# Optimization experiments

Measured on AMD Instinct MI355X. Metric: run time of the kernel, lower is better.

## Reference

```python
import jax, jax.numpy as jnp
import numpy as np

N_PROP, N_GRID, N_KEY, C_FEAT = 128, 216, 4096, 128
RADII = (0.8, 1.6)
NSAMPLES = (16, 16)
C_OUT = 64  # per-branch MLP output channels


def setup_inputs() -> dict:
    key = jax.random.key(0)
    ks = jax.random.split(key, 20)
    s = 0.05
    return {
        "wlh": jax.random.uniform(ks[0], (N_PROP, 3)) * 4.0 + 0.5,
        "center": jax.random.normal(ks[1], (N_PROP, 3)) * 5.0,
        "yaw": jax.random.uniform(ks[2], (N_PROP,)) * 2.0 * np.pi,
        "u": jax.random.uniform(ks[3], (N_PROP, N_GRID, 3)),
        "keypoints_xyz": jax.random.normal(ks[4], (1, N_KEY, 3)) * 5.0,
        "keypoints_features": jax.random.normal(ks[5], (1, C_FEAT, N_KEY)),
        "pn0_w1": jax.random.normal(ks[6], (C_OUT, C_FEAT + 3)) * s,
        "pn0_g1": jnp.ones((C_OUT,)), "pn0_b1": jnp.zeros((C_OUT,)),
        "pn0_w2": jax.random.normal(ks[7], (C_OUT, C_OUT)) * s,
        "pn0_g2": jnp.ones((C_OUT,)), "pn0_b2": jnp.zeros((C_OUT,)),
        "pn1_w1": jax.random.normal(ks[8], (C_OUT, C_FEAT + 3)) * s,
        "pn1_g1": jnp.ones((C_OUT,)), "pn1_b1": jnp.zeros((C_OUT,)),
        "pn1_w2": jax.random.normal(ks[9], (C_OUT, C_OUT)) * s,
        "pn1_g2": jnp.ones((C_OUT,)), "pn1_b2": jnp.zeros((C_OUT,)),
        "red_w1": jax.random.normal(ks[10], (256, N_GRID * 2 * C_OUT)) * 0.01,
        "red_b1": jnp.zeros((256,)),
        "red_w2": jax.random.normal(ks[11], (256, 256)) * s,
        "red_b2": jnp.zeros((256,)),
    }


def reference(wlh, center, yaw, u, keypoints_xyz, keypoints_features,
              pn0_w1, pn0_g1, pn0_b1, pn0_w2, pn0_g2, pn0_b2,
              pn1_w1, pn1_g1, pn1_b1, pn1_w2, pn1_g2, pn1_b2,
              red_w1, red_b1, red_w2, red_b2):
    n, m, _ = u.shape
    # --- sample gridpoints inside proposals and rotate by yaw around z ---
    gp = u * wlh[:, None, :]                                 # (n, m, 3)
    c, s = jnp.cos(yaw), jnp.sin(yaw)
    R = jnp.stack([c, -s, s, c], axis=-1).reshape(-1, 2, 2)   # (n, 2, 2)
    xy = jnp.einsum('njk,nmk->nmj', R, gp[..., :2])
    grid = jnp.concatenate([xy, gp[..., 2:]], -1) + center[:, None, :]
    grid = grid.reshape(-1, 3)                               # (G, 3), G = n*m

    kp = keypoints_xyz[0]                                    # (K, 3)
    kf = jnp.transpose(keypoints_features[0])                # (K, C)
    K = kp.shape[0]

    # squared distances (G, K) without materializing (G, K, 3)
    d2 = (jnp.sum(grid * grid, -1)[:, None]
          + jnp.sum(kp * kp, -1)[None, :]
          - 2.0 * grid @ kp.T)

    def ball_query(radius, nsample):
        # first `nsample` in-radius indices in original order; pad with first
        # hit; all-zeros if no point in radius (pointnet2 CUDA semantics).
        mask = d2 < radius * radius
        cand = jnp.where(mask, jnp.arange(K, dtype=jnp.int32), K)
        srt = jnp.sort(cand, axis=-1)[:, :nsample]           # (G, ns)
        first = srt[:, :1]
        return jnp.where(srt < K, srt, jnp.where(first < K, first, 0))

    def branch(radius, nsample, w1, g1, b1, w2, g2, b2):
        idx = ball_query(radius, nsample)                    # (G, ns)
        xyz = kp[idx] - grid[:, None, :]                     # (G, ns, 3)
        x = jnp.concatenate([xyz, kf[idx]], -1)              # (G, ns, 3+C)
        h = jax.nn.relu(jnp.einsum('gnc,oc->gno', x, w1) * g1 + b1)
        h = jax.nn.relu(jnp.einsum('gnc,oc->gno', h, w2) * g2 + b2)
        return jnp.max(h, axis=1)                            # (G, C_OUT)

    f0 = branch(RADII[0], NSAMPLES[0], pn0_w1, pn0_g1, pn0_b1, pn0_w2, pn0_g2, pn0_b2)
    f1 = branch(RADII[1], NSAMPLES[1], pn1_w1, pn1_g1, pn1_b1, pn1_w2, pn1_g2, pn1_b2)
    pooled = jnp.concatenate([f0, f1], -1)                   # (G, 2*C_OUT)
    Cp = pooled.shape[-1]

    # faithful replication of (1,C,n,m).permute(0,3,1,2).view(1,n,-1)
    t = pooled.reshape(n, m, Cp)                             # gridpoint order (n, m)
    red_in = jnp.transpose(t, (1, 2, 0)).reshape(1, n, m * Cp)

    h = jax.nn.relu(red_in @ red_w1.T + red_b1)
    return jax.nn.relu(h @ red_w2.T + red_b2)                # (1, n, 256)
```

## Files before the change

kernel.cpp:

```cpp
#include <hip/hip_runtime.h>
#include <hip/hip_bf16.h>

typedef unsigned short u16;
typedef unsigned int   u32;
typedef unsigned long long u64;

#define N_PROPC 128
#define N_GRIDC 216
#define G_TOT   27648
#define N_KEYC  4096
#define C_FEATC 128
#define R0SQ    0.64f
#define R1SQ    2.56f
#define BF16_ONES_DWORD 0x3F803F80u

typedef __attribute__((ext_vector_type(8))) short bf16x8;
typedef __attribute__((ext_vector_type(4))) float f32x4;

#if __has_builtin(__builtin_amdgcn_fcmpf)
#define BALLOT_LT(a, b) __builtin_amdgcn_fcmpf((a), (b), 4)
#else
#define BALLOT_LT(a, b) __ballot((a) < (b))
#endif

__device__ __forceinline__ float bf2f(u16 u) {
    return __uint_as_float(((u32)u) << 16);
}
__device__ __forceinline__ u16 f2bf(float f) {
    u32 u = __float_as_uint(f);
    u32 r = (u + 0x7fffu + ((u >> 16) & 1u)) >> 16;
    return (u16)r;
}
__device__ __forceinline__ bool is_bf16(const u32* flagp) {
    return *flagp == BF16_ONES_DWORD;
}
__device__ __forceinline__ float ld(const void* p, int i, bool bf) {
    return bf ? bf2f(((const u16*)p)[i]) : ((const float*)p)[i];
}
__device__ __forceinline__ u16 ldb(const void* p, int i, bool bf) {
    return bf ? ((const u16*)p)[i] : f2bf(((const float*)p)[i]);
}

__global__ __launch_bounds__(256) void prep_fused_kernel(
    const u32* __restrict__ flagp,
    const void* __restrict__ kxyz,
    const void* __restrict__ wlh, const void* __restrict__ center,
    const void* __restrict__ yaw, const void* __restrict__ uu,
    const void* __restrict__ kf,
    const void* __restrict__ w10, const void* __restrict__ g10, const void* __restrict__ b10,
    const void* __restrict__ w20, const void* __restrict__ g20, const void* __restrict__ b20,
    const void* __restrict__ w11, const void* __restrict__ g11, const void* __restrict__ b11,
    const void* __restrict__ w21, const void* __restrict__ g21, const void* __restrict__ b21,
    const void* __restrict__ rw2,
    float4* __restrict__ kp4, float4* __restrict__ grid4, u16* __restrict__ kfT,
    u16* __restrict__ w1mf, u16* __restrict__ w2mf,
    float* __restrict__ g1f, float* __restrict__ b1f,
    float* __restrict__ g2f, float* __restrict__ b2f,
    float* __restrict__ w2rT)
{
    const bool bf = is_bf16(flagp);
    const int bid = blockIdx.x, tid = threadIdx.x;

    if (bid < 16) {
        int k = bid * 256 + tid;
        float x = ld(kxyz, k*3, bf), y = ld(kxyz, k*3+1, bf), z = ld(kxyz, k*3+2, bf);
        kp4[k] = make_float4(x, y, z, 0.0f);
    } else if (bid < 124) {
        int g = (bid - 16) * 256 + tid;
        int n = g / N_GRIDC;
        float ux = ld(uu, g*3, bf), uy = ld(uu, g*3+1, bf), uz = ld(uu, g*3+2, bf);
        float gpx = ux * ld(wlh, n*3, bf);
        float gpy = uy * ld(wlh, n*3+1, bf);
        float gpz = uz * ld(wlh, n*3+2, bf);
        float yv = ld(yaw, n, bf);
        float c = cosf(yv), sn = sinf(yv);
        float x = (c*gpx - sn*gpy) + ld(center, n*3, bf);
        float y = (sn*gpx + c*gpy) + ld(center, n*3+1, bf);
        float z = gpz + ld(center, n*3+2, bf);
        grid4[g] = make_float4(x, y, z, 0.0f);
    } else if (bid < 2172) {
        int t = (bid - 124) * 256 + tid;
        int key = t >> 7, feat = t & 127;
        kfT[t] = ldb(kf, feat * N_KEYC + key, bf);
    } else if (bid < 2174) {
        const int b = bid - 2172;
        const void* w1 = b ? w11 : w10; const void* g1v = b ? g11 : g10;
        const void* w2 = b ? w21 : w20; const void* g2v = b ? g21 : g20;
        const void* b1v = b ? b11 : b10; const void* b2v = b ? b21 : b20;
        for (int f = tid; f < 10240; f += 256) {
            int j = f & 7, t1 = f >> 3;
            int n = t1 & 15, t2 = t1 >> 4;
            int quad = t2 & 3, t3 = t2 >> 2;
            int kt = t3 % 5, nt = t3 / 5;
            int k = kt*32 + quad*8 + j;
            int o = nt*16 + n;
            u16 v = 0;
            if (k < 128)      v = ldb(w1, o*131 + 3 + k, bf);
            else if (k < 131) v = ldb(w1, o*131 + (k - 128), bf);
            w1mf[b*10240 + f] = v;
        }
        for (int f = tid; f < 4096; f += 256) {
            int j = f & 7, t1 = f >> 3;
            int n = t1 & 15, t2 = t1 >> 4;
            int quad = t2 & 3, t3 = t2 >> 2;
            int kt = t3 & 1, nt = t3 >> 1;
            int k = kt*32 + quad*8 + j;
            int o = nt*16 + n;
            w2mf[b*4096 + f] = ldb(w2, o*64 + k, bf);
        }
        if (tid < 64) {
            g1f[b*64 + tid] = ld(g1v, tid, bf);
            b1f[b*64 + tid] = ld(b1v, tid, bf);
            g2f[b*64 + tid] = ld(g2v, tid, bf);
            b2f[b*64 + tid] = ld(b2v, tid, bf);
        }
    } else {
        int t = (bid - 2174) * 256 + tid;
        int o = t & 255, c = t >> 8;
        w2rT[c*256 + o] = ld(rw2, o*256 + c, bf);
    }
}

__global__ __launch_bounds__(256) void ballquery_kernel(
    const float4* __restrict__ kp4,
    const float4* __restrict__ grid4, u16* __restrict__ idx01)
{
    __shared__ __attribute__((aligned(16))) float4 sk[2048];
    const int tid = threadIdx.x;
    const int lane = tid & 63;
    const int wid = tid >> 6;
    const int g0 = blockIdx.x * 16 + wid * 4;
    const float4 gra = grid4[g0];
    const float4 grb = grid4[g0 + 1];
    const float4 grc = grid4[g0 + 2];
    const float4 grd = grid4[g0 + 3];

    u64 m0[4] = {0, 0, 0, 0};
    u64 m1[4] = {0, 0, 0, 0};
    #pragma unroll 1
    for (int pass = 0; pass < 2; ++pass) {
        if (pass) __syncthreads();
        for (int t = tid; t < 2048; t += 256) sk[t] = kp4[pass*2048 + t];
        __syncthreads();
        #pragma unroll
        for (int it = 0; it < 32; ++it) {
            const float4 kv = sk[it*64 + lane];
            const int chunk = pass*32 + it;
            float dx, dy, dz, d;
            dx = kv.x - gra.x; dy = kv.y - gra.y; dz = kv.z - gra.z;
            d = fmaf(dx, dx, fmaf(dy, dy, dz * dz));
            const u64 a1 = BALLOT_LT(d, R1SQ); const u64 a0 = BALLOT_LT(d, R0SQ);
            dx = kv.x - grb.x; dy = kv.y - grb.y; dz = kv.z - grb.z;
            d = fmaf(dx, dx, fmaf(dy, dy, dz * dz));
            const u64 b1m = BALLOT_LT(d, R1SQ); const u64 b0m = BALLOT_LT(d, R0SQ);
            dx = kv.x - grc.x; dy = kv.y - grc.y; dz = kv.z - grc.z;
            d = fmaf(dx, dx, fmaf(dy, dy, dz * dz));
            const u64 c1m = BALLOT_LT(d, R1SQ); const u64 c0m = BALLOT_LT(d, R0SQ);
            dx = kv.x - grd.x; dy = kv.y - grd.y; dz = kv.z - grd.z;
            d = fmaf(dx, dx, fmaf(dy, dy, dz * dz));
            const u64 d1m = BALLOT_LT(d, R1SQ); const u64 d0m = BALLOT_LT(d, R0SQ);
            if (lane == chunk) {
                m1[0] = a1; m0[0] = a0;
                m1[1] = b1m; m0[1] = b0m;
                m1[2] = c1m; m0[2] = c0m;
                m1[3] = d1m; m0[3] = d0m;
            }
        }
    }

    #pragma unroll
    for (int gg = 0; gg < 4; ++gg) {
        const int g = g0 + gg;
        u16* o0 = idx01 + (size_t)g * 16;
        u16* o1 = idx01 + (size_t)G_TOT * 16 + (size_t)g * 16;
        #pragma unroll
        for (int rad = 0; rad < 2; ++rad) {
            u64 mask = rad ? m1[gg] : m0[gg];
            u16* op = rad ? o1 : o0;
            const int cnt = __popcll(mask);
            int inc = cnt;
            #pragma unroll
            for (int d = 1; d < 64; d <<= 1) {
                int t = __shfl_up(inc, d);
                if (lane >= d) inc += t;
            }
            const int pre = inc - cnt;
            int firstk = (cnt > 0 && pre == 0) ? (lane*64 + __ffsll(mask) - 1) : 0x7FFFFFFF;
            #pragma unroll
            for (int d = 32; d >= 1; d >>= 1)
                firstk = min(firstk, __shfl_xor(firstk, d));
            const int total = __shfl(inc, 63);
            u64 mrem = mask;
            int p = pre;
            while (mrem != 0 && p < 16) {
                int j = __ffsll(mrem) - 1;
                op[p] = (u16)(lane*64 + j);
                mrem &= mrem - 1;
                ++p;
            }
            if (lane < 16 && lane >= total)
                op[lane] = (u16)(firstk == 0x7FFFFFFF ? 0 : firstk);
        }
    }
}

__global__ __launch_bounds__(256) void pointnet_mfma_kernel(
    const float4* __restrict__ grid4, const float4* __restrict__ kp4,
    const u16* __restrict__ kfT,
    const u16* __restrict__ w1mf, const u16* __restrict__ w2mf,
    const float* __restrict__ g1f, const float* __restrict__ b1f,
    const float* __restrict__ g2f, const float* __restrict__ b2f,
    const u16* __restrict__ idx01, u16* __restrict__ ATb)
{
    __shared__ __attribute__((aligned(16))) u16 w1s[10240];
    __shared__ __attribute__((aligned(16))) u16 w2s[4096];
    __shared__ __attribute__((aligned(16))) u16 h1s[4][16*72];
    const int tid = threadIdx.x;
    const int branch = blockIdx.y;

    {
        const uint4* s1 = (const uint4*)(w1mf + branch*10240);
        uint4* d1 = (uint4*)w1s;
        for (int t = tid; t < 1280; t += 256) d1[t] = s1[t];
        const uint4* s2 = (const uint4*)(w2mf + branch*4096);
        uint4* d2 = (uint4*)w2s;
        for (int t = tid; t < 512; t += 256) d2[t] = s2[t];
    }
    __syncthreads();

    const int wid = tid >> 6, lane = tid & 63;
    const int n = lane & 15, quad = lane >> 4;
    const int mi = blockIdx.x % N_GRIDC;
    const int nig = blockIdx.x / N_GRIDC;
    const int ni0 = nig*16 + wid*4;

    float g1v[4], b1v[4], g2v[4], b2v[4];
    #pragma unroll
    for (int nt = 0; nt < 4; ++nt) {
        g1v[nt] = g1f[branch*64 + nt*16 + n];
        b1v[nt] = b1f[branch*64 + nt*16 + n];
        g2v[nt] = g2f[branch*64 + nt*16 + n];
        b2v[nt] = b2f[branch*64 + nt*16 + n];
    }

    int idxv[4];
    #pragma unroll
    for (int gg = 0; gg < 4; ++gg) {
        const int g = (ni0 + gg) * N_GRIDC + mi;
        idxv[gg] = idx01[(size_t)branch*(G_TOT*16) + g*16 + n] & (N_KEYC - 1);
    }

    u16* __restrict__ h1w = &h1s[wid][0];

    #pragma unroll 1
    for (int gg = 0; gg < 4; ++gg) {
        const int ni = ni0 + gg;
        const int g = ni * N_GRIDC + mi;
        const int idx = idxv[gg];
        const float4 kp = kp4[idx];
        const float4 gr = grid4[g];

        bf16x8 axyz = (bf16x8)(short)0;
        if (quad == 0) {
            axyz[0] = (short)f2bf(kp.x - gr.x);
            axyz[1] = (short)f2bf(kp.y - gr.y);
            axyz[2] = (short)f2bf(kp.z - gr.z);
        }

        f32x4 acc0 = {0.f,0.f,0.f,0.f}, acc1 = acc0, acc2_ = acc0, acc3 = acc0;
        f32x4* acc[4] = {&acc0, &acc1, &acc2_, &acc3};

        const u16* __restrict__ arow = kfT + idx * C_FEATC;
        #pragma unroll
        for (int kt = 0; kt < 4; ++kt) {
            uint4 araw = *(const uint4*)(arow + kt*32 + quad*8);
            bf16x8 a;
            __builtin_memcpy(&a, &araw, 16);
            #pragma unroll
            for (int nt = 0; nt < 4; ++nt) {
                bf16x8 b = *(const bf16x8*)&w1s[(((nt*5 + kt)*4 + quad)*16 + n)*8];
                *acc[nt] = __builtin_amdgcn_mfma_f32_16x16x32_bf16(a, b, *acc[nt], 0, 0, 0);
            }
        }
        #pragma unroll
        for (int nt = 0; nt < 4; ++nt) {
            bf16x8 b = *(const bf16x8*)&w1s[(((nt*5 + 4)*4 + quad)*16 + n)*8];
            *acc[nt] = __builtin_amdgcn_mfma_f32_16x16x32_bf16(axyz, b, *acc[nt], 0, 0, 0);
        }

        #pragma unroll
        for (int nt = 0; nt < 4; ++nt) {
            #pragma unroll
            for (int r = 0; r < 4; ++r) {
                float v = fmaxf(fmaf((*acc[nt])[r], g1v[nt], b1v[nt]), 0.0f);
                h1w[(quad*4 + r)*72 + nt*16 + n] = f2bf(v);
            }
        }

        f32x4 c0 = {0.f,0.f,0.f,0.f}, c1 = c0, c2 = c0, c3 = c0;
        f32x4* acc2[4] = {&c0, &c1, &c2, &c3};
        #pragma unroll
        for (int kt = 0; kt < 2; ++kt) {
            bf16x8 a2 = *(const bf16x8*)&h1w[n*72 + kt*32 + quad*8];
            #pragma unroll
            for (int nt = 0; nt < 4; ++nt) {
                bf16x8 b = *(const bf16x8*)&w2s[(((nt*2 + kt)*4 + quad)*16 + n)*8];
                *acc2[nt] = __builtin_amdgcn_mfma_f32_16x16x32_bf16(a2, b, *acc2[nt], 0, 0, 0);
            }
        }

        #pragma unroll
        for (int nt = 0; nt < 4; ++nt) {
            float v0 = fmaxf(fmaf((*acc2[nt])[0], g2v[nt], b2v[nt]), 0.0f);
            float v1 = fmaxf(fmaf((*acc2[nt])[1], g2v[nt], b2v[nt]), 0.0f);
            float v2 = fmaxf(fmaf((*acc2[nt])[2], g2v[nt], b2v[nt]), 0.0f);
            float v3 = fmaxf(fmaf((*acc2[nt])[3], g2v[nt], b2v[nt]), 0.0f);
            float v = fmaxf(fmaxf(v0, v1), fmaxf(v2, v3));
            v = fmaxf(v, __shfl_xor(v, 16));
            v = fmaxf(v, __shfl_xor(v, 32));
            if (lane < 16) {
                const int ci = branch*64 + nt*16 + n;
                const int flat = mi*16384 + ci*128 + ni;
                ATb[flat] = f2bf(v);
            }
        }
    }
}

__global__ __launch_bounds__(256) void red1_mfma_kernel(
    const u32* __restrict__ flagp,
    const u16* __restrict__ ATb, const void* __restrict__ rw1,
    float* __restrict__ part)
{
    const bool bf = is_bf16(flagp);
    const int tid = threadIdx.x;
    const int wid = tid >> 6, lane = tid & 63;
    const int w = blockIdx.x * 4 + wid;
    const int kc = w & 15;
    const int nt = (w >> 4) & 15;
    const int mt = w >> 8;
    const int n = lane & 15, quad = lane >> 4;
    const int o = nt*16 + n;

    const u16* __restrict__ arow = ATb + (size_t)(mt*16 + n) * 27648;

    f32x4 acc = {0.f, 0.f, 0.f, 0.f};
    if (bf) {
        const u16* __restrict__ brow = (const u16*)rw1 + (size_t)o * 27648;
        #pragma unroll 2
        for (int s = 0; s < 54; ++s) {
            const int kk = kc*54 + s;
            uint4 araw = *(const uint4*)(arow + kk*32 + quad*8);
            bf16x8 a;
            __builtin_memcpy(&a, &araw, 16);
            uint4 braw = *(const uint4*)(brow + kk*32 + quad*8);
            bf16x8 b;
            __builtin_memcpy(&b, &braw, 16);
            acc = __builtin_amdgcn_mfma_f32_16x16x32_bf16(a, b, acc, 0, 0, 0);
        }
    } else {
        const float* __restrict__ brow = (const float*)rw1 + (size_t)o * 27648;
        #pragma unroll 2
        for (int s = 0; s < 54; ++s) {
            const int kk = kc*54 + s;
            uint4 araw = *(const uint4*)(arow + kk*32 + quad*8);
            bf16x8 a;
            __builtin_memcpy(&a, &araw, 16);
            const float4 f0 = *(const float4*)(brow + kk*32 + quad*8);
            const float4 f1 = *(const float4*)(brow + kk*32 + quad*8 + 4);
            bf16x8 b;
            b[0] = (short)f2bf(f0.x); b[1] = (short)f2bf(f0.y);
            b[2] = (short)f2bf(f0.z); b[3] = (short)f2bf(f0.w);
            b[4] = (short)f2bf(f1.x); b[5] = (short)f2bf(f1.y);
            b[6] = (short)f2bf(f1.z); b[7] = (short)f2bf(f1.w);
            acc = __builtin_amdgcn_mfma_f32_16x16x32_bf16(a, b, acc, 0, 0, 0);
        }
    }
    #pragma unroll
    for (int r = 0; r < 4; ++r) {
        const int i = mt*16 + quad*4 + r;
        part[kc*32768 + i*256 + nt*16 + n] = acc[r];
    }
}

__global__ __launch_bounds__(256) void tail_kernel(
    const u32* __restrict__ flagp,
    const float* __restrict__ part, const void* __restrict__ rb1,
    const float* __restrict__ w2rT, const void* __restrict__ rb2,
    void* __restrict__ outp)
{
    __shared__ float hs[256];
    const bool bf = is_bf16(flagp);
    const int o = threadIdx.x, i = blockIdx.x;
    float s = ld(rb1, o, bf);
    #pragma unroll
    for (int kc = 0; kc < 16; ++kc) s += part[kc*32768 + i*256 + o];
    hs[o] = fmaxf(s, 0.0f);
    __syncthreads();
    float s2 = ld(rb2, o, bf);
    #pragma unroll 8
    for (int c = 0; c < 256; ++c)
        s2 = fmaf(hs[c], w2rT[c*256 + o], s2);
    float v = fmaxf(s2, 0.0f);
    if (bf) ((u16*)outp)[i*256 + o] = f2bf(v);
    else    ((float*)outp)[i*256 + o] = v;
}


extern "C" void kernel_launch(void* const* d_in, const int* in_sizes, int n_in,
                              void* d_out, int out_size, void* d_ws, size_t ws_size,
                              hipStream_t stream) {
    const void* wlh    = d_in[0];
    const void* center = d_in[1];
    const void* yaw    = d_in[2];
    const void* uu     = d_in[3];
    const void* kxyz   = d_in[4];
    const void* kfeat  = d_in[5];
    const void* p0w1 = d_in[6];  const void* p0g1 = d_in[7];
    const void* p0b1 = d_in[8];  const void* p0w2 = d_in[9];
    const void* p0g2 = d_in[10]; const void* p0b2 = d_in[11];
    const void* p1w1 = d_in[12]; const void* p1g1 = d_in[13];
    const void* p1b1 = d_in[14]; const void* p1w2 = d_in[15];
    const void* p1g2 = d_in[16]; const void* p1b2 = d_in[17];
    const void* rw1 = d_in[18];
    const void* rb1 = d_in[19];
    const void* rw2 = d_in[20];
    const void* rb2 = d_in[21];
    const u32* flagp = (const u32*)d_in[7];

    char* w = (char*)d_ws;
    float4* kp4   = (float4*)(w + 65536);
    float4* grid4 = (float4*)(w + 131072);
    u16*    kfT   = (u16*)(w + 573440);
    u16*    w1mf  = (u16*)(w + 1622016);
    u16*    w2mf  = (u16*)(w + 1662976);
    float*  g1f   = (float*)(w + 1679360);
    float*  b1f   = (float*)(w + 1679872);
    float*  g2f   = (float*)(w + 1680384);
    float*  b2f   = (float*)(w + 1680896);
    float*  w2rT  = (float*)(w + 1721856);
    u16*    idx01 = (u16*)(w + 1984000);
    u16*    ATb   = (u16*)(w + 3754496);
    float*  part  = (float*)(w + 32066048);

    prep_fused_kernel<<<2430, 256, 0, stream>>>(flagp,
        kxyz, wlh, center, yaw, uu, kfeat,
        p0w1, p0g1, p0b1, p0w2, p0g2, p0b2,
        p1w1, p1g1, p1b1, p1w2, p1g2, p1b2,
        rw2,
        kp4, grid4, kfT,
        w1mf, w2mf, g1f, b1f, g2f, b2f, w2rT);

    ballquery_kernel<<<G_TOT/16, 256, 0, stream>>>(kp4, grid4, idx01);

    dim3 pngrid(G_TOT/16, 2);
    pointnet_mfma_kernel<<<pngrid, 256, 0, stream>>>(grid4, kp4, kfT, w1mf, w2mf,
                                                     g1f, b1f, g2f, b2f, idx01, ATb);

    red1_mfma_kernel<<<512, 256, 0, stream>>>(flagp, ATb, rw1, part);
    tail_kernel<<<128, 256, 0, stream>>>(flagp, part, rb1, w2rT, rb2, d_out);
}
```

Before: 284.2 us.

## Process two gridpoints per iteration in pointnet and regroup red1 waves to share B rows

The pointnet kernel now handles two gridpoints per loop iteration. It issues both gathered feature-row loads up front and interleaves two independent MFMA chains, which hides gather latency and MFMA dependency stalls, at the cost of more registers and a doubled per-wave LDS scratch. The red1 kernel remaps waves so the four waves in a block share the same kc/nt (the same weight rows) and cover different M tiles, improving cache reuse of the large red_w1 matrix.

```diff
diff --git a/kernel.cpp b/kernel.cpp
--- a/kernel.cpp
+++ b/kernel.cpp
@@ -214,7 +214,7 @@
 {
     __shared__ __attribute__((aligned(16))) u16 w1s[10240];
     __shared__ __attribute__((aligned(16))) u16 w2s[4096];
-    __shared__ __attribute__((aligned(16))) u16 h1s[4][16*72];
+    __shared__ __attribute__((aligned(16))) u16 h1s[4][32*72];
     const int tid = threadIdx.x;
     const int branch = blockIdx.y;
 
@@ -253,75 +253,106 @@
     u16* __restrict__ h1w = &h1s[wid][0];
 
     #pragma unroll 1
-    for (int gg = 0; gg < 4; ++gg) {
-        const int ni = ni0 + gg;
-        const int g = ni * N_GRIDC + mi;
-        const int idx = idxv[gg];
-        const float4 kp = kp4[idx];
-        const float4 gr = grid4[g];
-
-        bf16x8 axyz = (bf16x8)(short)0;
+    for (int p = 0; p < 2; ++p) {
+        const int niA = ni0 + 2*p, niB = niA + 1;
+        const int idxA = idxv[2*p], idxB = idxv[2*p + 1];
+        const float4 kpA = kp4[idxA];
+        const float4 kpB = kp4[idxB];
+        const float4 grA = grid4[niA * N_GRIDC + mi];
+        const float4 grB = grid4[niB * N_GRIDC + mi];
+
+        const u16* __restrict__ arowA = kfT + idxA * C_FEATC;
+        const u16* __restrict__ arowB = kfT + idxB * C_FEATC;
+        uint4 arA[4], arB[4];
+        #pragma unroll
+        for (int kt = 0; kt < 4; ++kt) {
+            arA[kt] = *(const uint4*)(arowA + kt*32 + quad*8);
+            arB[kt] = *(const uint4*)(arowB + kt*32 + quad*8);
+        }
+
+        bf16x8 axyzA = (bf16x8)(short)0, axyzB = (bf16x8)(short)0;
         if (quad == 0) {
-            axyz[0] = (short)f2bf(kp.x - gr.x);
-            axyz[1] = (short)f2bf(kp.y - gr.y);
-            axyz[2] = (short)f2bf(kp.z - gr.z);
-        }
-
-        f32x4 acc0 = {0.f,0.f,0.f,0.f}, acc1 = acc0, acc2_ = acc0, acc3 = acc0;
-        f32x4* acc[4] = {&acc0, &acc1, &acc2_, &acc3};
-
-        const u16* __restrict__ arow = kfT + idx * C_FEATC;
+            axyzA[0] = (short)f2bf(kpA.x - grA.x);
+            axyzA[1] = (short)f2bf(kpA.y - grA.y);
+            axyzA[2] = (short)f2bf(kpA.z - grA.z);
+            axyzB[0] = (short)f2bf(kpB.x - grB.x);
+            axyzB[1] = (short)f2bf(kpB.y - grB.y);
+            axyzB[2] = (short)f2bf(kpB.z - grB.z);
+        }
+
+        f32x4 accA[4], accB[4];
+        #pragma unroll
+        for (int nt = 0; nt < 4; ++nt) {
+            accA[nt] = (f32x4){0.f, 0.f, 0.f, 0.f};
+            accB[nt] = (f32x4){0.f, 0.f, 0.f, 0.f};
+        }
+
         #pragma unroll
         for (int kt = 0; kt < 4; ++kt) {
-            uint4 araw = *(const uint4*)(arow + kt*32 + quad*8);
-            bf16x8 a;
-            __builtin_memcpy(&a, &araw, 16);
+            bf16x8 aA, aB;
+            __builtin_memcpy(&aA, &arA[kt], 16);
+            __builtin_memcpy(&aB, &arB[kt], 16);
             #pragma unroll
             for (int nt = 0; nt < 4; ++nt) {
                 bf16x8 b = *(const bf16x8*)&w1s[(((nt*5 + kt)*4 + quad)*16 + n)*8];
-                *acc[nt] = __builtin_amdgcn_mfma_f32_16x16x32_bf16(a, b, *acc[nt], 0, 0, 0);
+                accA[nt] = __builtin_amdgcn_mfma_f32_16x16x32_bf16(aA, b, accA[nt], 0, 0, 0);
+                accB[nt] = __builtin_amdgcn_mfma_f32_16x16x32_bf16(aB, b, accB[nt], 0, 0, 0);
             }
         }
         #pragma unroll
         for (int nt = 0; nt < 4; ++nt) {
             bf16x8 b = *(const bf16x8*)&w1s[(((nt*5 + 4)*4 + quad)*16 + n)*8];
-            *acc[nt] = __builtin_amdgcn_mfma_f32_16x16x32_bf16(axyz, b, *acc[nt], 0, 0, 0);
+            accA[nt] = __builtin_amdgcn_mfma_f32_16x16x32_bf16(axyzA, b, accA[nt], 0, 0, 0);
+            accB[nt] = __builtin_amdgcn_mfma_f32_16x16x32_bf16(axyzB, b, accB[nt], 0, 0, 0);
         }
 
         #pragma unroll
         for (int nt = 0; nt < 4; ++nt) {
             #pragma unroll
             for (int r = 0; r < 4; ++r) {
-                float v = fmaxf(fmaf((*acc[nt])[r], g1v[nt], b1v[nt]), 0.0f);
-                h1w[(quad*4 + r)*72 + nt*16 + n] = f2bf(v);
-            }
-        }
-
-        f32x4 c0 = {0.f,0.f,0.f,0.f}, c1 = c0, c2 = c0, c3 = c0;
-        f32x4* acc2[4] = {&c0, &c1, &c2, &c3};
+                float vA = fmaxf(fmaf(accA[nt][r], g1v[nt], b1v[nt]), 0.0f);
+                float vB = fmaxf(fmaf(accB[nt][r], g1v[nt], b1v[nt]), 0.0f);
+                h1w[(quad*4 + r)*72 + nt*16 + n] = f2bf(vA);
+                h1w[(16 + quad*4 + r)*72 + nt*16 + n] = f2bf(vB);
+            }
+        }
+
+        f32x4 cA[4], cB[4];
+        #pragma unroll
+        for (int nt = 0; nt < 4; ++nt) {
+            cA[nt] = (f32x4){0.f, 0.f, 0.f, 0.f};
+            cB[nt] = (f32x4){0.f, 0.f, 0.f, 0.f};
+        }
         #pragma unroll
         for (int kt = 0; kt < 2; ++kt) {
-            bf16x8 a2 = *(const bf16x8*)&h1w[n*72 + kt*32 + quad*8];
+            bf16x8 a2A = *(const bf16x8*)&h1w[n*72 + kt*32 + quad*8];
+            bf16x8 a2B = *(const bf16x8*)&h1w[(16 + n)*72 + kt*32 + quad*8];
             #pragma unroll
             for (int nt = 0; nt < 4; ++nt) {
                 bf16x8 b = *(const bf16x8*)&w2s[(((nt*2 + kt)*4 + quad)*16 + n)*8];
-                *acc2[nt] = __builtin_amdgcn_mfma_f32_16x16x32_bf16(a2, b, *acc2[nt], 0, 0, 0);
+                cA[nt] = __builtin_amdgcn_mfma_f32_16x16x32_bf16(a2A, b, cA[nt], 0, 0, 0);
+                cB[nt] = __builtin_amdgcn_mfma_f32_16x16x32_bf16(a2B, b, cB[nt], 0, 0, 0);
             }
         }
 
         #pragma unroll
         for (int nt = 0; nt < 4; ++nt) {
-            float v0 = fmaxf(fmaf((*acc2[nt])[0], g2v[nt], b2v[nt]), 0.0f);
-            float v1 = fmaxf(fmaf((*acc2[nt])[1], g2v[nt], b2v[nt]), 0.0f);
-            float v2 = fmaxf(fmaf((*acc2[nt])[2], g2v[nt], b2v[nt]), 0.0f);
-            float v3 = fmaxf(fmaf((*acc2[nt])[3], g2v[nt], b2v[nt]), 0.0f);
-            float v = fmaxf(fmaxf(v0, v1), fmaxf(v2, v3));
-            v = fmaxf(v, __shfl_xor(v, 16));
-            v = fmaxf(v, __shfl_xor(v, 32));
+            float vA = fmaxf(fmaxf(fmaxf(fmaf(cA[nt][0], g2v[nt], b2v[nt]), 0.0f),
+                                   fmaxf(fmaf(cA[nt][1], g2v[nt], b2v[nt]), 0.0f)),
+                             fmaxf(fmaxf(fmaf(cA[nt][2], g2v[nt], b2v[nt]), 0.0f),
+                                   fmaxf(fmaf(cA[nt][3], g2v[nt], b2v[nt]), 0.0f)));
+            float vB = fmaxf(fmaxf(fmaxf(fmaf(cB[nt][0], g2v[nt], b2v[nt]), 0.0f),
+                                   fmaxf(fmaf(cB[nt][1], g2v[nt], b2v[nt]), 0.0f)),
+                             fmaxf(fmaxf(fmaf(cB[nt][2], g2v[nt], b2v[nt]), 0.0f),
+                                   fmaxf(fmaf(cB[nt][3], g2v[nt], b2v[nt]), 0.0f)));
+            vA = fmaxf(vA, __shfl_xor(vA, 16));
+            vA = fmaxf(vA, __shfl_xor(vA, 32));
+            vB = fmaxf(vB, __shfl_xor(vB, 16));
+            vB = fmaxf(vB, __shfl_xor(vB, 32));
             if (lane < 16) {
                 const int ci = branch*64 + nt*16 + n;
-                const int flat = mi*16384 + ci*128 + ni;
-                ATb[flat] = f2bf(v);
+                ATb[mi*16384 + ci*128 + niA] = f2bf(vA);
+                ATb[mi*16384 + ci*128 + niB] = f2bf(vB);
             }
         }
     }
@@ -335,10 +366,10 @@
     const bool bf = is_bf16(flagp);
     const int tid = threadIdx.x;
     const int wid = tid >> 6, lane = tid & 63;
-    const int w = blockIdx.x * 4 + wid;
-    const int kc = w & 15;
-    const int nt = (w >> 4) & 15;
-    const int mt = w >> 8;
+    const int b = blockIdx.x;
+    const int kc = b & 15;
+    const int nt = (b >> 4) & 15;
+    const int mt = (b >> 8) * 4 + wid;
     const int n = lane & 15, quad = lane >> 4;
     const int o = nt*16 + n;
 
@@ -354,9 +385,9 @@
             bf16x8 a;
             __builtin_memcpy(&a, &araw, 16);
             uint4 braw = *(const uint4*)(brow + kk*32 + quad*8);
-            bf16x8 b;
-            __builtin_memcpy(&b, &braw, 16);
-            acc = __builtin_amdgcn_mfma_f32_16x16x32_bf16(a, b, acc, 0, 0, 0);
+            bf16x8 bb;
+            __builtin_memcpy(&bb, &braw, 16);
+            acc = __builtin_amdgcn_mfma_f32_16x16x32_bf16(a, bb, acc, 0, 0, 0);
         }
     } else {
         const float* __restrict__ brow = (const float*)rw1 + (size_t)o * 27648;
@@ -368,12 +399,12 @@
             __builtin_memcpy(&a, &araw, 16);
             const float4 f0 = *(const float4*)(brow + kk*32 + quad*8);
             const float4 f1 = *(const float4*)(brow + kk*32 + quad*8 + 4);
-            bf16x8 b;
-            b[0] = (short)f2bf(f0.x); b[1] = (short)f2bf(f0.y);
-            b[2] = (short)f2bf(f0.z); b[3] = (short)f2bf(f0.w);
-            b[4] = (short)f2bf(f1.x); b[5] = (short)f2bf(f1.y);
-            b[6] = (short)f2bf(f1.z); b[7] = (short)f2bf(f1.w);
-            acc = __builtin_amdgcn_mfma_f32_16x16x32_bf16(a, b, acc, 0, 0, 0);
+            bf16x8 bb;
+            bb[0] = (short)f2bf(f0.x); bb[1] = (short)f2bf(f0.y);
+            bb[2] = (short)f2bf(f0.z); bb[3] = (short)f2bf(f0.w);
+            bb[4] = (short)f2bf(f1.x); bb[5] = (short)f2bf(f1.y);
+            bb[6] = (short)f2bf(f1.z); bb[7] = (short)f2bf(f1.w);
+            acc = __builtin_amdgcn_mfma_f32_16x16x32_bf16(a, bb, acc, 0, 0, 0);
         }
     }
     #pragma unroll
```

Result: faster. 275.3 us (-3.1%).
